# Optimization experiments

Hardware: AMD Instinct MI355X
Metric: run time of the kernel (lower is better)

Reference implementation:

```python
import jax, jax.numpy as jnp
import numpy as np

S, B, D, H, DFF = 1024, 8, 1024, 16, 4096
HD = D // H
EPS = 1e-5


def layernorm(x, g, b):
    m = jnp.mean(x, axis=-1, keepdims=True)
    v = jnp.mean(jnp.square(x - m), axis=-1, keepdims=True)
    return (x - m) * jax.lax.rsqrt(v + EPS) * g + b


def setup_inputs() -> dict:
    key = jax.random.key(0)
    ks = jax.random.split(key, 6)
    w = 0.02
    return {
        "src": jax.random.normal(ks[0], (S, B, D), dtype=jnp.float32),
        "in_proj_w": jax.random.normal(ks[1], (3 * D, D), dtype=jnp.float32) * w,
        "in_proj_b": jnp.zeros((3 * D,), dtype=jnp.float32),
        "out_w": jax.random.normal(ks[2], (D, D), dtype=jnp.float32) * w,
        "out_b": jnp.zeros((D,), dtype=jnp.float32),
        "lin1_w": jax.random.normal(ks[3], (DFF, D), dtype=jnp.float32) * w,
        "lin1_b": jnp.zeros((DFF,), dtype=jnp.float32),
        "lin2_w": jax.random.normal(ks[4], (D, DFF), dtype=jnp.float32) * w,
        "lin2_b": jnp.zeros((D,), dtype=jnp.float32),
        "n1_g": jnp.ones((D,), dtype=jnp.float32),
        "n1_b": jnp.zeros((D,), dtype=jnp.float32),
        "n2_g": jnp.ones((D,), dtype=jnp.float32),
        "n2_b": jnp.zeros((D,), dtype=jnp.float32),
    }


def reference(src, in_proj_w, in_proj_b, out_w, out_b,
              lin1_w, lin1_b, lin2_w, lin2_b,
              n1_g, n1_b, n2_g, n2_b):
    # self-attention block (eval mode: dropout = identity)
    qkv = jnp.einsum('sbd,ed->sbe', src, in_proj_w) + in_proj_b  # [S,B,3D]
    q, k, v = jnp.split(qkv, 3, axis=-1)
    q = q.reshape(S, B, H, HD) * (1.0 / np.sqrt(HD)).astype(np.float32)
    k = k.reshape(S, B, H, HD)
    v = v.reshape(S, B, H, HD)
    scores = jnp.einsum('sbhd,tbhd->bhst', q, k)        # [B,H,S,S]
    attn = jax.nn.softmax(scores, axis=-1)
    o = jnp.einsum('bhst,tbhd->sbhd', attn, v).reshape(S, B, D)
    o = jnp.einsum('sbd,ed->sbe', o, out_w) + out_b
    # post-LN residuals
    x = layernorm(src + o, n1_g, n1_b)
    h = jax.nn.relu(jnp.einsum('sbd,fd->sbf', x, lin1_w) + lin1_b)
    f = jnp.einsum('sbf,df->sbd', h, lin2_w) + lin2_b
    return layernorm(x + f, n2_g, n2_b)
```

## Files before the change

kernel.cpp:

```cpp
#include <hip/hip_runtime.h>
#include <cstdint>
#include <cstddef>

#define S_  1024
#define B_  8
#define D_  1024
#define H_  16
#define HD_ 64
#define DFF_ 4096
#define M_  (S_*B_)
#define QKV_N (3*D_)

typedef float f32x4 __attribute__((ext_vector_type(4)));
typedef __bf16 bf16x8 __attribute__((ext_vector_type(8)));
typedef __bf16 bf16x4 __attribute__((ext_vector_type(4)));

#define GLDS16(gp, lp) __builtin_amdgcn_global_load_lds( \
    (__attribute__((address_space(1))) void*)(gp), \
    (__attribute__((address_space(3))) void*)(lp), 16, 0, 0)

#define CB0 (M_*D_/4)
#define CB1 (CB0 + QKV_N*D_/4)
#define CB2 (CB1 + D_*D_/4)
#define CB3 (CB2 + DFF_*D_/4)
#define CB4 (CB3 + D_*DFF_/4)

__global__ __launch_bounds__(256)
void cvt_all(const float* __restrict__ src, const float* __restrict__ w1f,
             const float* __restrict__ w2f, const float* __restrict__ w3f,
             const float* __restrict__ w4f,
             __bf16* __restrict__ src_bf, __bf16* __restrict__ w1,
             __bf16* __restrict__ w2, __bf16* __restrict__ w3,
             __bf16* __restrict__ w4)
{
    int i = blockIdx.x * 256 + threadIdx.x;
    const float* in; __bf16* out; int off;
    if      (i < CB0) { in = src; out = src_bf; off = 0;   }
    else if (i < CB1) { in = w1f; out = w1;     off = CB0; }
    else if (i < CB2) { in = w2f; out = w2;     off = CB1; }
    else if (i < CB3) { in = w3f; out = w3;     off = CB2; }
    else if (i < CB4) { in = w4f; out = w4;     off = CB3; }
    else return;
    int j = i - off;
    float4 v = *(const float4*)(in + (size_t)j * 4);
    __bf16 t[4] = {(__bf16)v.x, (__bf16)v.y, (__bf16)v.z, (__bf16)v.w};
    *(uint2*)(out + (size_t)j * 4) = *(uint2*)t;
}

template<bool OUT_BF16, bool RELU, bool ADD_BIAS, bool SPLITZ>
__global__ __launch_bounds__(512, 2)
void gemm256(const __bf16* __restrict__ A, const __bf16* __restrict__ W,
             const float* __restrict__ bias,
             void* __restrict__ Cv0, void* __restrict__ Cv1,
             int N, int Kloop, int lda)
{
    extern __shared__ __bf16 lds[];

    const int tid  = threadIdx.x;
    const int lane = tid & 63;
    const int wv   = tid >> 6;
    const int quad = lane >> 4;
    const int l15  = lane & 15;
    const int wm   = (wv >> 2) * 128;
    const int wn   = (wv & 3) * 64;

    const int id  = blockIdx.y * gridDim.x + blockIdx.x;
    const int nwg = gridDim.x * gridDim.y;
    const int q8  = nwg >> 3;
    const int k   = (id & 7) * q8 + (id >> 3);
    const int within = k & 31;
    const int chunk  = k >> 5;
    const int nchm   = gridDim.x >> 3;
    const int cm     = chunk % nchm;
    const int cn     = chunk / nchm;
    const int m0 = (cm * 8 + (within & 7)) * 256;
    const int n0 = (cn * 4 + (within >> 3)) * 256;

    void* Cv = Cv0;
    if (SPLITZ) {
        const int koff = blockIdx.z * Kloop;
        A += koff;
        W += koff;
        if (blockIdx.z) Cv = Cv1;
    }

    const int nt = Kloop >> 5;

    const int crow = tid >> 2;
    const int csl  = (tid & 3) ^ ((crow >> 1) & 3);
    const __bf16* gA0 = A + (size_t)(m0 + crow) * lda + csl * 8;
    const __bf16* gA1 = gA0 + (size_t)128 * lda;
    const __bf16* gW0 = W + (size_t)(n0 + crow) * lda + csl * 8;
    const __bf16* gW1 = gW0 + (size_t)128 * lda;
    char* ldsSt = (char*)lds + tid * 16;

    #define STAGE(kt, buf) do { \
        const int ko = (kt) << 5; \
        char* d_ = ldsSt + (buf) * 32768; \
        GLDS16(gW0 + ko, d_ + 16384); \
        GLDS16(gW1 + ko, d_ + 24576); \
        GLDS16(gA0 + ko, d_); \
        GLDS16(gA1 + ko, d_ + 8192); \
    } while (0)

    const int swz = (quad ^ ((l15 >> 1) & 3)) * 8;
    const __bf16* aBase = lds + (wm + l15) * 32 + swz;
    const __bf16* bBase = lds + 8192 + (wn + l15) * 32 + swz;

    #define RDA_ALL(arr, buf) do { const __bf16* p_ = aBase + (buf) * 16384; \
        _Pragma("unroll") for (int i_ = 0; i_ < 8; ++i_) \
            arr[i_] = *(const bf16x8*)(p_ + i_ * 512); } while (0)
    #define RDB_ALL(arr, buf) do { const __bf16* p_ = bBase + (buf) * 16384; \
        _Pragma("unroll") for (int j_ = 0; j_ < 4; ++j_) \
            arr[j_] = *(const bf16x8*)(p_ + j_ * 512); } while (0)

    #define BARRIER_DRAIN() do { \
        asm volatile("s_waitcnt vmcnt(0)" ::: "memory"); \
        __builtin_amdgcn_s_barrier(); \
        __builtin_amdgcn_sched_barrier(0); \
    } while (0)

    STAGE(0, 0);
    STAGE(1, 1);
    BARRIER_DRAIN();

    f32x4 acc[8][4] = {};
    bf16x8 aP[8], aN[8], b_[4];

    RDA_ALL(aP, 0);

    int b_cur = 0;
    for (int t = 0; t < nt; t += 2) {
        int b_nxt = b_cur + 1; if (b_nxt == 3) b_nxt = 0;
        int b_st  = b_nxt + 1; if (b_st  == 3) b_st  = 0;

        if (t + 2 < nt) STAGE(t + 2, b_st);
        RDB_ALL(b_, b_cur);
        RDA_ALL(aN, b_nxt);
        __builtin_amdgcn_s_setprio(1);
        #pragma unroll
        for (int i = 0; i < 8; ++i)
            #pragma unroll
            for (int j = 0; j < 4; ++j)
                acc[i][j] = __builtin_amdgcn_mfma_f32_16x16x32_bf16(aP[i], b_[j], acc[i][j], 0, 0, 0);
        __builtin_amdgcn_s_setprio(0);
        BARRIER_DRAIN();

        if (t + 3 < nt) STAGE(t + 3, b_cur);
        RDB_ALL(b_, b_nxt);
        if (t + 2 < nt) RDA_ALL(aP, b_st);
        __builtin_amdgcn_s_setprio(1);
        #pragma unroll
        for (int i = 0; i < 8; ++i)
            #pragma unroll
            for (int j = 0; j < 4; ++j)
                acc[i][j] = __builtin_amdgcn_mfma_f32_16x16x32_bf16(aN[i], b_[j], acc[i][j], 0, 0, 0);
        __builtin_amdgcn_s_setprio(0);
        if (t + 2 < nt) BARRIER_DRAIN();

        b_cur = b_st;
    }

    #undef BARRIER_DRAIN
    #undef RDA_ALL
    #undef RDB_ALL
    #undef STAGE

    float bvj[4];
    #pragma unroll
    for (int j = 0; j < 4; ++j)
        bvj[j] = ADD_BIAS ? bias[n0 + wn + j * 16 + l15] : 0.f;
    const size_t cbase = (size_t)(m0 + wm + quad * 4) * N + (n0 + wn + l15);
    #pragma unroll
    for (int i = 0; i < 8; ++i) {
        #pragma unroll
        for (int r = 0; r < 4; ++r) {
            const size_t rowb = cbase + (size_t)(i * 16 + r) * N;
            #pragma unroll
            for (int j = 0; j < 4; ++j) {
                float v = acc[i][j][r] + bvj[j];
                if (RELU) v = fmaxf(v, 0.f);
                if (OUT_BF16)
                    ((__bf16*)Cv)[rowb + j * 16] = (__bf16)v;
                else
                    ((float*)Cv)[rowb + j * 16] = v;
            }
        }
    }
}

__global__ __launch_bounds__(256)
void v_transpose(const __bf16* __restrict__ qkv, __bf16* __restrict__ vt)
{
    __shared__ __bf16 T[64 * 65];
    const int tid = threadIdx.x;
    const int t0  = blockIdx.x * 64;
    const int bh  = blockIdx.y;
    const int b   = bh & (B_ - 1);
    const int h   = bh / B_;

    #pragma unroll
    for (int j = 0; j < 2; ++j) {
        int c = j * 256 + tid;
        int i = c >> 3, cc = c & 7;
        const __bf16* g = qkv + (size_t)((t0 + i) * B_ + b) * QKV_N + 2 * D_ + h * HD_ + cc * 8;
        bf16x8 v = *(const bf16x8*)g;
        #pragma unroll
        for (int u = 0; u < 8; ++u) T[(cc * 8 + u) * 65 + i] = v[u];
    }
    __syncthreads();
    #pragma unroll
    for (int j = 0; j < 2; ++j) {
        int c = j * 256 + tid;
        int d = c >> 3, cc = c & 7;
        __bf16 pk[8];
        #pragma unroll
        for (int u = 0; u < 8; ++u) pk[u] = T[d * 65 + cc * 8 + u];
        *(uint4*)(vt + ((size_t)bh * HD_ + d) * S_ + t0 + cc * 8) = *(uint4*)pk;
    }
}

#define AST 64

__global__ __launch_bounds__(512, 6)
void attn_flash(const __bf16* __restrict__ qkv, const __bf16* __restrict__ vt,
                __bf16* __restrict__ out)
{
    __shared__ __bf16 Ks[2][64 * AST];
    __shared__ __bf16 Vs[2][64 * AST];
    __shared__ __bf16 Ps[128 * AST];

    const int tid  = threadIdx.x;
    const int lane = tid & 63;
    const int wv   = tid >> 6;
    const int quad = lane >> 4;
    const int l15  = lane & 15;

    const int id = blockIdx.y * gridDim.x + blockIdx.x;
    const int k  = (id & 7) * ((S_ / 128) * B_ * H_ / 8) + (id >> 3);
    const int s0 = (k & 7) * 128;
    const int bh = k >> 3;
    const int b  = bh & (B_ - 1);
    const int h  = bh / B_;

    {
        int i = tid >> 3, cc = tid & 7;
        int scc = cc ^ (i & 7);
        GLDS16(qkv + (size_t)(i * B_ + b) * QKV_N + D_ + h * HD_ + scc * 8,
               (char*)(Ks[0]) + tid * 16);
        GLDS16(vt + ((size_t)bh * HD_ + i) * S_ + scc * 8,
               (char*)(Vs[0]) + tid * 16);
    }

    const int qrow = wv * 16 + l15;
    bf16x8 bq[2];
    #pragma unroll
    for (int kk = 0; kk < 2; ++kk)
        bq[kk] = *(const bf16x8*)(qkv + (size_t)((s0 + qrow) * B_ + b) * QKV_N
                                  + h * HD_ + kk * 32 + quad * 8);

    __syncthreads();

    f32x4 oacc[4] = {};
    float m_run = -1e30f, l_run = 0.f;
    const float C2    = 0.125f * 1.44269504f;
    const float LOG2E = 1.44269504f;

    const int nt = S_ / 64;
    for (int it = 0; it < nt; ++it) {
        const int cur = it & 1;

        if (it + 1 < nt) {
            const int t1 = (it + 1) * 64;
            int i = tid >> 3, cc = tid & 7;
            int scc = cc ^ (i & 7);
            GLDS16(qkv + (size_t)((t1 + i) * B_ + b) * QKV_N + D_ + h * HD_ + scc * 8,
                   (char*)(Ks[cur ^ 1]) + tid * 16);
            GLDS16(vt + ((size_t)bh * HD_ + i) * S_ + t1 + scc * 8,
                   (char*)(Vs[cur ^ 1]) + tid * 16);
        }

        f32x4 sacc[4] = {};
        #pragma unroll
        for (int kk = 0; kk < 2; ++kk) {
            #pragma unroll
            for (int j = 0; j < 4; ++j) {
                int krow = j * 16 + l15;
                bf16x8 ak = *(const bf16x8*)(&Ks[cur][krow * AST + (((kk * 4 + quad) ^ (krow & 7)) * 8)]);
                sacc[j] = __builtin_amdgcn_mfma_f32_16x16x32_bf16(ak, bq[kk], sacc[j], 0, 0, 0);
            }
        }

        float mx = sacc[0][0];
        #pragma unroll
        for (int j = 0; j < 4; ++j)
            #pragma unroll
            for (int r = 0; r < 4; ++r) mx = fmaxf(mx, sacc[j][r]);
        mx = fmaxf(mx, __shfl_xor(mx, 16, 64));
        mx = fmaxf(mx, __shfl_xor(mx, 32, 64));
        float pm = mx * 0.125f;

        if (!__all(pm - m_run <= 8.0f)) {
            float mnew  = fmaxf(m_run, pm);
            float alpha = __builtin_amdgcn_exp2f((m_run - mnew) * LOG2E);
            l_run *= alpha;
            #pragma unroll
            for (int r = 0; r < 4; ++r) {
                float ar = __shfl(alpha, quad * 4 + r, 64);
                #pragma unroll
                for (int jd = 0; jd < 4; ++jd) oacc[jd][r] *= ar;
            }
            m_run = mnew;
        }

        float k1 = m_run * LOG2E;
        float rs = 0.f;
        #pragma unroll
        for (int j = 0; j < 4; ++j)
            #pragma unroll
            for (int r = 0; r < 4; ++r) {
                float p = __builtin_amdgcn_exp2f(sacc[j][r] * C2 - k1);
                sacc[j][r] = p;
                rs += p;
            }
        rs += __shfl_xor(rs, 16, 64);
        rs += __shfl_xor(rs, 32, 64);
        l_run += rs;

        #pragma unroll
        for (int j = 0; j < 4; ++j) {
            __bf16 pk[4] = {(__bf16)sacc[j][0], (__bf16)sacc[j][1],
                            (__bf16)sacc[j][2], (__bf16)sacc[j][3]};
            int s16 = (j * 2 + (quad >> 1)) ^ (qrow & 7);
            *(uint2*)(Ps + qrow * AST + s16 * 8 + (quad & 1) * 4) = *(uint2*)pk;
        }

        #pragma unroll
        for (int kk = 0; kk < 2; ++kk) {
            bf16x8 ap = *(const bf16x8*)(Ps + qrow * AST + (((kk * 4 + quad) ^ (qrow & 7)) * 8));
            #pragma unroll
            for (int jd = 0; jd < 4; ++jd) {
                int vrow = jd * 16 + l15;
                bf16x8 bv = *(const bf16x8*)(&Vs[cur][vrow * AST + (((kk * 4 + quad) ^ (vrow & 7)) * 8)]);
                oacc[jd] = __builtin_amdgcn_mfma_f32_16x16x32_bf16(ap, bv, oacc[jd], 0, 0, 0);
            }
        }

        __syncthreads();
    }

    float linv = 1.f / l_run;
    #pragma unroll
    for (int r = 0; r < 4; ++r) {
        float lr = __shfl(linv, quad * 4 + r, 64);
        int s = s0 + wv * 16 + quad * 4 + r;
        #pragma unroll
        for (int jd = 0; jd < 4; ++jd) {
            int d = jd * 16 + l15;
            out[(size_t)(s * B_ + b) * D_ + h * HD_ + d] = (__bf16)(oacc[jd][r] * lr);
        }
    }
}

__global__ __launch_bounds__(256)
void ln_res3(const float* __restrict__ xa, const __bf16* __restrict__ p0,
             const __bf16* __restrict__ p1, const float* __restrict__ bias,
             const float* __restrict__ g, const float* __restrict__ beta,
             float* __restrict__ yout, __bf16* __restrict__ ybf)
{
    __shared__ float red[8];
    const int row = blockIdx.x;
    const int tid = threadIdx.x;
    const size_t base = (size_t)row * D_ + tid * 4;

    float4 a  = *(const float4*)(xa + base);
    bf16x4 q0 = *(const bf16x4*)(p0 + base);
    bf16x4 q1 = *(const bf16x4*)(p1 + base);
    float4 bb = *(const float4*)(bias + tid * 4);
    float x0 = a.x + (float)q0[0] + (float)q1[0] + bb.x;
    float x1 = a.y + (float)q0[1] + (float)q1[1] + bb.y;
    float x2 = a.z + (float)q0[2] + (float)q1[2] + bb.z;
    float x3 = a.w + (float)q0[3] + (float)q1[3] + bb.w;

    float s  = x0 + x1 + x2 + x3;
    float ss = x0 * x0 + x1 * x1 + x2 * x2 + x3 * x3;
    for (int msk = 1; msk <= 32; msk <<= 1) {
        s  += __shfl_xor(s,  msk, 64);
        ss += __shfl_xor(ss, msk, 64);
    }
    const int wv = tid >> 6;
    if ((tid & 63) == 0) { red[wv] = s; red[4 + wv] = ss; }
    __syncthreads();
    s  = red[0] + red[1] + red[2] + red[3];
    ss = red[4] + red[5] + red[6] + red[7];
    float mean = s * (1.f / D_);
    float var  = ss * (1.f / D_) - mean * mean;
    float rstd = rsqrtf(var + 1e-5f);

    float4 gv = *(const float4*)(g + tid * 4);
    float4 bv = *(const float4*)(beta + tid * 4);
    float y0 = (x0 - mean) * rstd * gv.x + bv.x;
    float y1 = (x1 - mean) * rstd * gv.y + bv.y;
    float y2 = (x2 - mean) * rstd * gv.z + bv.z;
    float y3 = (x3 - mean) * rstd * gv.w + bv.w;
    *(float4*)(yout + base) = make_float4(y0, y1, y2, y3);
    if (ybf) {
        __bf16 t[4] = {(__bf16)y0, (__bf16)y1, (__bf16)y2, (__bf16)y3};
        *(uint2*)(ybf + base) = *(uint2*)t;
    }
}

extern "C" void kernel_launch(void* const* d_in, const int* in_sizes, int n_in,
                              void* d_out, int out_size, void* d_ws, size_t ws_size,
                              hipStream_t stream)
{
    const float* src       = (const float*)d_in[0];
    const float* in_proj_w = (const float*)d_in[1];
    const float* in_proj_b = (const float*)d_in[2];
    const float* out_w     = (const float*)d_in[3];
    const float* out_b     = (const float*)d_in[4];
    const float* lin1_w    = (const float*)d_in[5];
    const float* lin1_b    = (const float*)d_in[6];
    const float* lin2_w    = (const float*)d_in[7];
    const float* lin2_b    = (const float*)d_in[8];
    const float* n1_g = (const float*)d_in[9];
    const float* n1_b = (const float*)d_in[10];
    const float* n2_g = (const float*)d_in[11];
    const float* n2_b = (const float*)d_in[12];

    char* ws = (char*)d_ws;
    size_t off = 0;
    auto alloc = [&](size_t bytes) { char* p = ws + off; off += (bytes + 255) & ~(size_t)255; return p; };

    __bf16* src_bf = (__bf16*)alloc((size_t)M_ * D_ * 2);
    __bf16* w1     = (__bf16*)alloc((size_t)QKV_N * D_ * 2);
    __bf16* w2     = (__bf16*)alloc((size_t)D_ * D_ * 2);
    __bf16* w3     = (__bf16*)alloc((size_t)DFF_ * D_ * 2);
    __bf16* w4     = (__bf16*)alloc((size_t)D_ * DFF_ * 2);
    __bf16* qkv    = (__bf16*)alloc((size_t)M_ * QKV_N * 2);
    char*   h_r    = alloc((size_t)M_ * DFF_ * 2);
    __bf16* xbf    = (__bf16*)alloc((size_t)M_ * D_ * 2);
    float*  xf     = (float*)alloc((size_t)M_ * D_ * 4);
    __bf16* vt     = (__bf16*)alloc((size_t)B_ * H_ * HD_ * S_ * 2);

    const size_t PART = (size_t)M_ * D_;
    __bf16* attn_o = src_bf;
    __bf16* o0 = (__bf16*)h_r;
    __bf16* o1 = o0 + PART;
    __bf16* hbf = (__bf16*)h_r;
    __bf16* f0 = vt;
    __bf16* f1 = xbf;

    const size_t SHM = 98304;

    cvt_all<<<(CB4 + 255) / 256, 256, 0, stream>>>(
        src, in_proj_w, out_w, lin1_w, lin2_w, src_bf, w1, w2, w3, w4);

    gemm256<true, false, true, false><<<dim3(M_ / 256, QKV_N / 256), 512, SHM, stream>>>(
        src_bf, w1, in_proj_b, qkv, nullptr, QKV_N, D_, D_);

    v_transpose<<<dim3(S_ / 64, B_ * H_), 256, 0, stream>>>(qkv, vt);

    attn_flash<<<dim3(S_ / 128, B_ * H_), 512, 0, stream>>>(qkv, vt, attn_o);

    gemm256<true, false, false, true><<<dim3(M_ / 256, D_ / 256, 2), 512, SHM, stream>>>(
        attn_o, w2, nullptr, o0, o1, D_, D_ / 2, D_);

    ln_res3<<<M_, 256, 0, stream>>>(src, o0, o1, out_b, n1_g, n1_b, xf, xbf);

    gemm256<true, true, true, false><<<dim3(M_ / 256, DFF_ / 256), 512, SHM, stream>>>(
        xbf, w3, lin1_b, hbf, nullptr, DFF_, D_, D_);

    gemm256<true, false, false, true><<<dim3(M_ / 256, D_ / 256, 2), 512, SHM, stream>>>(
        hbf, w4, nullptr, f0, f1, D_, DFF_ / 2, DFF_);

    ln_res3<<<M_, 256, 0, stream>>>(xf, f0, f1, lin2_b, n2_g, n2_b, (float*)d_out, nullptr);
}
```

Before: 469.1 us.

## Shrink GEMM tile to 128x256 with simple double-buffered pipeline

Replaces the 256x256 GEMM tile (8 waves, each holding 128x64 of accumulators, triple-buffered LDS with A-fragment prefetch) with a 128x256 tile where each wave computes 64x64, using a plain two-stage LDS double buffer. LDS per block halves and launch bounds allow 4 blocks per CU, so more workgroups and occupancy become available to hide latency. In exchange, data reuse per loaded byte drops, global/LDS traffic per FLOP rises, and the software register prefetch of A fragments is gone.

```diff
diff --git a/kernel.cpp b/kernel.cpp
--- a/kernel.cpp
+++ b/kernel.cpp
@@ -48,8 +48,8 @@
 }
 
 template<bool OUT_BF16, bool RELU, bool ADD_BIAS, bool SPLITZ>
-__global__ __launch_bounds__(512, 2)
-void gemm256(const __bf16* __restrict__ A, const __bf16* __restrict__ W,
+__global__ __launch_bounds__(512, 4)
+void gemm128(const __bf16* __restrict__ A, const __bf16* __restrict__ W,
              const float* __restrict__ bias,
              void* __restrict__ Cv0, void* __restrict__ Cv1,
              int N, int Kloop, int lda)
@@ -61,8 +61,8 @@
     const int wv   = tid >> 6;
     const int quad = lane >> 4;
     const int l15  = lane & 15;
-    const int wm   = (wv >> 2) * 128;
-    const int wn   = (wv & 3) * 64;
+    const int wm   = (wv & 1) * 64;
+    const int wn   = (wv >> 1) * 64;
 
     const int id  = blockIdx.y * gridDim.x + blockIdx.x;
     const int nwg = gridDim.x * gridDim.y;
@@ -73,7 +73,7 @@
     const int nchm   = gridDim.x >> 3;
     const int cm     = chunk % nchm;
     const int cn     = chunk / nchm;
-    const int m0 = (cm * 8 + (within & 7)) * 256;
+    const int m0 = (cm * 8 + (within & 7)) * 128;
     const int n0 = (cn * 4 + (within >> 3)) * 256;
 
     void* Cv = Cv0;
@@ -89,30 +89,21 @@
     const int crow = tid >> 2;
     const int csl  = (tid & 3) ^ ((crow >> 1) & 3);
     const __bf16* gA0 = A + (size_t)(m0 + crow) * lda + csl * 8;
-    const __bf16* gA1 = gA0 + (size_t)128 * lda;
     const __bf16* gW0 = W + (size_t)(n0 + crow) * lda + csl * 8;
     const __bf16* gW1 = gW0 + (size_t)128 * lda;
     char* ldsSt = (char*)lds + tid * 16;
 
     #define STAGE(kt, buf) do { \
         const int ko = (kt) << 5; \
-        char* d_ = ldsSt + (buf) * 32768; \
-        GLDS16(gW0 + ko, d_ + 16384); \
-        GLDS16(gW1 + ko, d_ + 24576); \
+        char* d_ = ldsSt + (buf) * 24576; \
+        GLDS16(gW0 + ko, d_ + 8192); \
+        GLDS16(gW1 + ko, d_ + 16384); \
         GLDS16(gA0 + ko, d_); \
-        GLDS16(gA1 + ko, d_ + 8192); \
     } while (0)
 
     const int swz = (quad ^ ((l15 >> 1) & 3)) * 8;
     const __bf16* aBase = lds + (wm + l15) * 32 + swz;
-    const __bf16* bBase = lds + 8192 + (wn + l15) * 32 + swz;
-
-    #define RDA_ALL(arr, buf) do { const __bf16* p_ = aBase + (buf) * 16384; \
-        _Pragma("unroll") for (int i_ = 0; i_ < 8; ++i_) \
-            arr[i_] = *(const bf16x8*)(p_ + i_ * 512); } while (0)
-    #define RDB_ALL(arr, buf) do { const __bf16* p_ = bBase + (buf) * 16384; \
-        _Pragma("unroll") for (int j_ = 0; j_ < 4; ++j_) \
-            arr[j_] = *(const bf16x8*)(p_ + j_ * 512); } while (0)
+    const __bf16* bBase = lds + 4096 + (wn + l15) * 32 + swz;
 
     #define BARRIER_DRAIN() do { \
         asm volatile("s_waitcnt vmcnt(0)" ::: "memory"); \
@@ -121,49 +112,34 @@
     } while (0)
 
     STAGE(0, 0);
-    STAGE(1, 1);
     BARRIER_DRAIN();
 
-    f32x4 acc[8][4] = {};
-    bf16x8 aP[8], aN[8], b_[4];
-
-    RDA_ALL(aP, 0);
-
-    int b_cur = 0;
-    for (int t = 0; t < nt; t += 2) {
-        int b_nxt = b_cur + 1; if (b_nxt == 3) b_nxt = 0;
-        int b_st  = b_nxt + 1; if (b_st  == 3) b_st  = 0;
-
-        if (t + 2 < nt) STAGE(t + 2, b_st);
-        RDB_ALL(b_, b_cur);
-        RDA_ALL(aN, b_nxt);
+    f32x4 acc[4][4] = {};
+
+    for (int t = 0; t < nt; ++t) {
+        const int cur = t & 1;
+        if (t + 1 < nt) STAGE(t + 1, cur ^ 1);
+
+        const __bf16* aB = aBase + cur * 12288;
+        const __bf16* bB = bBase + cur * 12288;
+        bf16x8 b_[4];
+        #pragma unroll
+        for (int j = 0; j < 4; ++j)
+            b_[j] = *(const bf16x8*)(bB + j * 512);
         __builtin_amdgcn_s_setprio(1);
         #pragma unroll
-        for (int i = 0; i < 8; ++i)
+        for (int i = 0; i < 4; ++i) {
+            bf16x8 a_ = *(const bf16x8*)(aB + i * 512);
             #pragma unroll
             for (int j = 0; j < 4; ++j)
-                acc[i][j] = __builtin_amdgcn_mfma_f32_16x16x32_bf16(aP[i], b_[j], acc[i][j], 0, 0, 0);
+                acc[i][j] = __builtin_amdgcn_mfma_f32_16x16x32_bf16(a_, b_[j], acc[i][j], 0, 0, 0);
+        }
         __builtin_amdgcn_s_setprio(0);
-        BARRIER_DRAIN();
-
-        if (t + 3 < nt) STAGE(t + 3, b_cur);
-        RDB_ALL(b_, b_nxt);
-        if (t + 2 < nt) RDA_ALL(aP, b_st);
-        __builtin_amdgcn_s_setprio(1);
-        #pragma unroll
-        for (int i = 0; i < 8; ++i)
-            #pragma unroll
-            for (int j = 0; j < 4; ++j)
-                acc[i][j] = __builtin_amdgcn_mfma_f32_16x16x32_bf16(aN[i], b_[j], acc[i][j], 0, 0, 0);
-        __builtin_amdgcn_s_setprio(0);
-        if (t + 2 < nt) BARRIER_DRAIN();
-
-        b_cur = b_st;
+
+        if (t + 1 < nt) BARRIER_DRAIN();
     }
 
     #undef BARRIER_DRAIN
-    #undef RDA_ALL
-    #undef RDB_ALL
     #undef STAGE
 
     float bvj[4];
@@ -172,7 +148,7 @@
         bvj[j] = ADD_BIAS ? bias[n0 + wn + j * 16 + l15] : 0.f;
     const size_t cbase = (size_t)(m0 + wm + quad * 4) * N + (n0 + wn + l15);
     #pragma unroll
-    for (int i = 0; i < 8; ++i) {
+    for (int i = 0; i < 4; ++i) {
         #pragma unroll
         for (int r = 0; r < 4; ++r) {
             const size_t rowb = cbase + (size_t)(i * 16 + r) * N;
@@ -451,27 +427,27 @@
     __bf16* f0 = vt;
     __bf16* f1 = xbf;
 
-    const size_t SHM = 98304;
+    const size_t SHM = 49152;
 
     cvt_all<<<(CB4 + 255) / 256, 256, 0, stream>>>(
         src, in_proj_w, out_w, lin1_w, lin2_w, src_bf, w1, w2, w3, w4);
 
-    gemm256<true, false, true, false><<<dim3(M_ / 256, QKV_N / 256), 512, SHM, stream>>>(
+    gemm128<true, false, true, false><<<dim3(M_ / 128, QKV_N / 256), 512, SHM, stream>>>(
         src_bf, w1, in_proj_b, qkv, nullptr, QKV_N, D_, D_);
 
     v_transpose<<<dim3(S_ / 64, B_ * H_), 256, 0, stream>>>(qkv, vt);
 
     attn_flash<<<dim3(S_ / 128, B_ * H_), 512, 0, stream>>>(qkv, vt, attn_o);
 
-    gemm256<true, false, false, true><<<dim3(M_ / 256, D_ / 256, 2), 512, SHM, stream>>>(
+    gemm128<true, false, false, true><<<dim3(M_ / 128, D_ / 256, 2), 512, SHM, stream>>>(
         attn_o, w2, nullptr, o0, o1, D_, D_ / 2, D_);
 
     ln_res3<<<M_, 256, 0, stream>>>(src, o0, o1, out_b, n1_g, n1_b, xf, xbf);
 
-    gemm256<true, true, true, false><<<dim3(M_ / 256, DFF_ / 256), 512, SHM, stream>>>(
+    gemm128<true, true, true, false><<<dim3(M_ / 128, DFF_ / 256), 512, SHM, stream>>>(
         xbf, w3, lin1_b, hbf, nullptr, DFF_, D_, D_);
 
-    gemm256<true, false, false, true><<<dim3(M_ / 256, D_ / 256, 2), 512, SHM, stream>>>(
+    gemm128<true, false, false, true><<<dim3(M_ / 128, D_ / 256, 2), 512, SHM, stream>>>(
         hbf, w4, nullptr, f0, f1, D_, DFF_ / 2, DFF_);
 
     ln_res3<<<M_, 256, 0, stream>>>(xf, f0, f1, lin2_b, n2_g, n2_b, (float*)d_out, nullptr);
```

Measured after the change: 482.8 us. +2.9%, slower.

## Stage 128-key K/V tiles per barrier in flash attention with dynamic LDS

Applied to the files above, without the earlier changes.

The attention loop now loads 128 keys of K and V per double-buffered stage and processes them as two 64-key sub-steps, which halves the number of __syncthreads barriers and loop iterations. V is stored in LDS with a 128-wide row and a 16-way XOR swizzle, and shared memory moves to an 80 KB dynamic allocation. Launch bounds drop from 6 to 4 waves-per-EU hint, reflecting the larger LDS footprint. The cost is lower occupancy in exchange for fewer synchronisations and more work between prefetches.

```diff
diff --git a/kernel.cpp b/kernel.cpp
--- a/kernel.cpp
+++ b/kernel.cpp
@@ -220,15 +220,14 @@
     }
 }
 
-#define AST 64
-
-__global__ __launch_bounds__(512, 6)
+__global__ __launch_bounds__(512, 4)
 void attn_flash(const __bf16* __restrict__ qkv, const __bf16* __restrict__ vt,
                 __bf16* __restrict__ out)
 {
-    __shared__ __bf16 Ks[2][64 * AST];
-    __shared__ __bf16 Vs[2][64 * AST];
-    __shared__ __bf16 Ps[128 * AST];
+    extern __shared__ __bf16 alds[];
+    __bf16* Ks0 = alds;
+    __bf16* Vs0 = alds + 16384;
+    __bf16* Ps  = alds + 32768;
 
     const int tid  = threadIdx.x;
     const int lane = tid & 63;
@@ -243,14 +242,25 @@
     const int b  = bh & (B_ - 1);
     const int h  = bh / B_;
 
-    {
-        int i = tid >> 3, cc = tid & 7;
-        int scc = cc ^ (i & 7);
-        GLDS16(qkv + (size_t)(i * B_ + b) * QKV_N + D_ + h * HD_ + scc * 8,
-               (char*)(Ks[0]) + tid * 16);
-        GLDS16(vt + ((size_t)bh * HD_ + i) * S_ + scc * 8,
-               (char*)(Vs[0]) + tid * 16);
-    }
+    const int i0k = tid >> 3, cck = tid & 7, scck = cck ^ (i0k & 7);
+    const int i0v = tid >> 4, ccv = tid & 15, sccv = ccv ^ (i0v & 15);
+    const __bf16* gK0 = qkv + ((size_t)i0k * B_ + b) * QKV_N + D_ + h * HD_ + scck * 8;
+    const __bf16* gK1 = gK0 + (size_t)64 * B_ * QKV_N;
+    const __bf16* gV0 = vt + ((size_t)bh * HD_ + i0v) * S_ + sccv * 8;
+    const __bf16* gV1 = gV0 + (size_t)32 * S_;
+    char* dK = (char*)Ks0 + tid * 16;
+    char* dV = (char*)Vs0 + tid * 16;
+    const size_t KADV = (size_t)128 * B_ * QKV_N;
+
+    #define STAGEKV(buf) do { \
+        GLDS16(gK0, dK + (buf) * 16384); \
+        GLDS16(gK1, dK + (buf) * 16384 + 8192); \
+        GLDS16(gV0, dV + (buf) * 16384); \
+        GLDS16(gV1, dV + (buf) * 16384 + 8192); \
+        gK0 += KADV; gK1 += KADV; gV0 += 128; gV1 += 128; \
+    } while (0)
+
+    STAGEKV(0);
 
     const int qrow = wv * 16 + l15;
     bf16x8 bq[2];
@@ -265,89 +275,86 @@
     float m_run = -1e30f, l_run = 0.f;
     const float C2    = 0.125f * 1.44269504f;
     const float LOG2E = 1.44269504f;
-
-    const int nt = S_ / 64;
-    for (int it = 0; it < nt; ++it) {
+    const int xk = l15 & 7;
+    const __bf16* psB = Ps + qrow * 64;
+
+    const int nt2 = S_ / 128;
+    for (int it = 0; it < nt2; ++it) {
         const int cur = it & 1;
-
-        if (it + 1 < nt) {
-            const int t1 = (it + 1) * 64;
-            int i = tid >> 3, cc = tid & 7;
-            int scc = cc ^ (i & 7);
-            GLDS16(qkv + (size_t)((t1 + i) * B_ + b) * QKV_N + D_ + h * HD_ + scc * 8,
-                   (char*)(Ks[cur ^ 1]) + tid * 16);
-            GLDS16(vt + ((size_t)bh * HD_ + i) * S_ + t1 + scc * 8,
-                   (char*)(Vs[cur ^ 1]) + tid * 16);
-        }
-
-        f32x4 sacc[4] = {};
-        #pragma unroll
-        for (int kk = 0; kk < 2; ++kk) {
+        if (it + 1 < nt2) STAGEKV(cur ^ 1);
+
+        #pragma unroll
+        for (int s = 0; s < 2; ++s) {
+            f32x4 sacc[4] = {};
+            #pragma unroll
+            for (int kk = 0; kk < 2; ++kk) {
+                const __bf16* akB = Ks0 + cur * 8192 + s * 4096 + l15 * 64
+                                    + (((kk * 4 + quad) ^ xk) * 8);
+                #pragma unroll
+                for (int j = 0; j < 4; ++j)
+                    sacc[j] = __builtin_amdgcn_mfma_f32_16x16x32_bf16(
+                        *(const bf16x8*)(akB + j * 1024), bq[kk], sacc[j], 0, 0, 0);
+            }
+
+            float mx = sacc[0][0];
+            #pragma unroll
+            for (int j = 0; j < 4; ++j)
+                #pragma unroll
+                for (int r = 0; r < 4; ++r) mx = fmaxf(mx, sacc[j][r]);
+            mx = fmaxf(mx, __shfl_xor(mx, 16, 64));
+            mx = fmaxf(mx, __shfl_xor(mx, 32, 64));
+            float pm = mx * 0.125f;
+
+            if (!__all(pm - m_run <= 8.0f)) {
+                float mnew  = fmaxf(m_run, pm);
+                float alpha = __builtin_amdgcn_exp2f((m_run - mnew) * LOG2E);
+                l_run *= alpha;
+                #pragma unroll
+                for (int r = 0; r < 4; ++r) {
+                    float ar = __shfl(alpha, quad * 4 + r, 64);
+                    #pragma unroll
+                    for (int jd = 0; jd < 4; ++jd) oacc[jd][r] *= ar;
+                }
+                m_run = mnew;
+            }
+
+            float k1 = m_run * LOG2E;
+            float rs = 0.f;
+            #pragma unroll
+            for (int j = 0; j < 4; ++j)
+                #pragma unroll
+                for (int r = 0; r < 4; ++r) {
+                    float p = __builtin_amdgcn_exp2f(sacc[j][r] * C2 - k1);
+                    sacc[j][r] = p;
+                    rs += p;
+                }
+            rs += __shfl_xor(rs, 16, 64);
+            rs += __shfl_xor(rs, 32, 64);
+            l_run += rs;
+
             #pragma unroll
             for (int j = 0; j < 4; ++j) {
-                int krow = j * 16 + l15;
-                bf16x8 ak = *(const bf16x8*)(&Ks[cur][krow * AST + (((kk * 4 + quad) ^ (krow & 7)) * 8)]);
-                sacc[j] = __builtin_amdgcn_mfma_f32_16x16x32_bf16(ak, bq[kk], sacc[j], 0, 0, 0);
+                __bf16 pk[4] = {(__bf16)sacc[j][0], (__bf16)sacc[j][1],
+                                (__bf16)sacc[j][2], (__bf16)sacc[j][3]};
+                int s16 = (j * 2 + (quad >> 1)) ^ xk;
+                *(uint2*)(psB + s16 * 8 + (quad & 1) * 4) = *(uint2*)pk;
+            }
+
+            #pragma unroll
+            for (int kk = 0; kk < 2; ++kk) {
+                bf16x8 ap = *(const bf16x8*)(psB + (((kk * 4 + quad) ^ xk) * 8));
+                const __bf16* bvB = Vs0 + cur * 8192 + l15 * 128
+                                    + (((s * 8 + kk * 4 + quad) ^ l15) * 8);
+                #pragma unroll
+                for (int jd = 0; jd < 4; ++jd)
+                    oacc[jd] = __builtin_amdgcn_mfma_f32_16x16x32_bf16(
+                        ap, *(const bf16x8*)(bvB + jd * 2048), oacc[jd], 0, 0, 0);
             }
         }
 
-        float mx = sacc[0][0];
-        #pragma unroll
-        for (int j = 0; j < 4; ++j)
-            #pragma unroll
-            for (int r = 0; r < 4; ++r) mx = fmaxf(mx, sacc[j][r]);
-        mx = fmaxf(mx, __shfl_xor(mx, 16, 64));
-        mx = fmaxf(mx, __shfl_xor(mx, 32, 64));
-        float pm = mx * 0.125f;
-
-        if (!__all(pm - m_run <= 8.0f)) {
-            float mnew  = fmaxf(m_run, pm);
-            float alpha = __builtin_amdgcn_exp2f((m_run - mnew) * LOG2E);
-            l_run *= alpha;
-            #pragma unroll
-            for (int r = 0; r < 4; ++r) {
-                float ar = __shfl(alpha, quad * 4 + r, 64);
-                #pragma unroll
-                for (int jd = 0; jd < 4; ++jd) oacc[jd][r] *= ar;
-            }
-            m_run = mnew;
-        }
-
-        float k1 = m_run * LOG2E;
-        float rs = 0.f;
-        #pragma unroll
-        for (int j = 0; j < 4; ++j)
-            #pragma unroll
-            for (int r = 0; r < 4; ++r) {
-                float p = __builtin_amdgcn_exp2f(sacc[j][r] * C2 - k1);
-                sacc[j][r] = p;
-                rs += p;
-            }
-        rs += __shfl_xor(rs, 16, 64);
-        rs += __shfl_xor(rs, 32, 64);
-        l_run += rs;
-
-        #pragma unroll
-        for (int j = 0; j < 4; ++j) {
-            __bf16 pk[4] = {(__bf16)sacc[j][0], (__bf16)sacc[j][1],
-                            (__bf16)sacc[j][2], (__bf16)sacc[j][3]};
-            int s16 = (j * 2 + (quad >> 1)) ^ (qrow & 7);
-            *(uint2*)(Ps + qrow * AST + s16 * 8 + (quad & 1) * 4) = *(uint2*)pk;
-        }
-
-        #pragma unroll
-        for (int kk = 0; kk < 2; ++kk) {
-            bf16x8 ap = *(const bf16x8*)(Ps + qrow * AST + (((kk * 4 + quad) ^ (qrow & 7)) * 8));
-            #pragma unroll
-            for (int jd = 0; jd < 4; ++jd) {
-                int vrow = jd * 16 + l15;
-                bf16x8 bv = *(const bf16x8*)(&Vs[cur][vrow * AST + (((kk * 4 + quad) ^ (vrow & 7)) * 8)]);
-                oacc[jd] = __builtin_amdgcn_mfma_f32_16x16x32_bf16(ap, bv, oacc[jd], 0, 0, 0);
-            }
-        }
-
         __syncthreads();
     }
+    #undef STAGEKV
 
     float linv = 1.f / l_run;
     #pragma unroll
@@ -451,7 +458,8 @@
     __bf16* f0 = vt;
     __bf16* f1 = xbf;
 
-    const size_t SHM = 98304;
+    const size_t SHM  = 98304;
+    const size_t ASHM = 81920;
 
     cvt_all<<<(CB4 + 255) / 256, 256, 0, stream>>>(
         src, in_proj_w, out_w, lin1_w, lin2_w, src_bf, w1, w2, w3, w4);
@@ -461,7 +469,7 @@
 
     v_transpose<<<dim3(S_ / 64, B_ * H_), 256, 0, stream>>>(qkv, vt);
 
-    attn_flash<<<dim3(S_ / 128, B_ * H_), 512, 0, stream>>>(qkv, vt, attn_o);
+    attn_flash<<<dim3(S_ / 128, B_ * H_), 512, ASHM, stream>>>(qkv, vt, attn_o);
 
     gemm256<true, false, false, true><<<dim3(M_ / 256, D_ / 256, 2), 512, SHM, stream>>>(
         attn_o, w2, nullptr, o0, o1, D_, D_ / 2, D_);
```

After: 457.0 us. -2.6%, faster.
